# Kernel tuning notes

Measured on AMD Instinct MI355X. Metric: run time of the kernel, lower is better.

Reference implementation:

```python
import jax, jax.numpy as jnp
import numpy as np

B, L, D_IN = 8, 512, 1024
HEAD_SIZE = 64
NUM_LABELS = 16
INF = 1e12


def _rotary_sin_cos(seq_len, dim):
    # HF RoFormerSinusoidalPositionalEmbedding: inv_freq = 10000^(-2i/dim)
    pos = np.arange(seq_len, dtype=np.float64)[:, None]
    inv_freq = 1.0 / np.power(10000.0, 2.0 * np.arange(dim // 2) / dim)
    ang = pos * inv_freq  # [L, dim//2]
    # interleave: [s0, s0, s1, s1, ...] (matches stack([sin,sin],-1).reshape)
    sin = jnp.asarray(np.repeat(np.sin(ang), 2, axis=-1), dtype=jnp.float32)
    cos = jnp.asarray(np.repeat(np.cos(ang), 2, axis=-1), dtype=jnp.float32)
    return sin[None], cos[None]  # [1, L, dim]


def _rotate_half(x):
    # [-x1, x0, -x3, x2, ...]
    return jnp.stack([-x[..., 1::2], x[..., ::2]], axis=-1).reshape(x.shape)


def setup_inputs() -> dict:
    key = jax.random.key(0)
    k1, k2, k3, k4, k5 = jax.random.split(key, 5)
    s1 = 1.0 / np.sqrt(D_IN)
    s2 = 1.0 / np.sqrt(2 * HEAD_SIZE)
    return {
        "inputs": jax.random.normal(k1, (B, L, D_IN), dtype=jnp.float32),
        "attention_mask": jnp.ones((B, L), dtype=jnp.int32),
        "W1": jax.random.uniform(k2, (D_IN, 2 * HEAD_SIZE), jnp.float32, -s1, s1),
        "b1": jax.random.uniform(k3, (2 * HEAD_SIZE,), jnp.float32, -s1, s1),
        "W2": jax.random.uniform(k4, (2 * HEAD_SIZE, 2 * NUM_LABELS), jnp.float32, -s2, s2),
        "b2": jax.random.uniform(k5, (2 * NUM_LABELS,), jnp.float32, -s2, s2),
    }


def reference(inputs, attention_mask, W1, b1, W2, b2):
    h = inputs @ W1 + b1                      # [B, L, 2*head_size]
    qw, kw = h[..., ::2], h[..., 1::2]        # [B, L, head_size]

    sin, cos = _rotary_sin_cos(h.shape[1], HEAD_SIZE)
    qw = qw * cos + _rotate_half(qw) * sin
    kw = kw * cos + _rotate_half(kw) * sin

    logits = jnp.einsum("bmd,bnd->bmn", qw, kw) / (HEAD_SIZE ** 0.5)  # [B, L, L]

    bias = (h @ W2 + b2).transpose(0, 2, 1) / 2.0        # [B, 2*heads, L]
    logits = logits[:, None] + bias[:, ::2, None, :] + bias[:, 1::2, :, None]  # [B, heads, L, L]

    am = attention_mask.astype(logits.dtype)
    attn_mask = 1.0 - am[:, None, None, :] * am[:, None, :, None]
    logits = logits - attn_mask * INF

    tril = jnp.tril(jnp.ones((h.shape[1], h.shape[1]), logits.dtype), k=-1)
    logits = logits - tril * INF
    return logits
```

## Files before the change

### kernel.cpp

```cpp
#include <hip/hip_runtime.h>
#include <math.h>

#define B_   8
#define L_   512
#define DIN  1024
#define H_   128
#define HEAD 64
#define NL   16
#define INF_ 1.0e12f

#define SIN_OFF  0
#define COS_OFF  (512*32)
#define QROT_OFF (COS_OFF + 512*32)
#define KROT_OFF (QROT_OFF + B_*L_*HEAD)
#define BQ_OFF   (KROT_OFF + B_*L_*HEAD)
#define BK_OFF   (BQ_OFF + B_*NL*L_)
#define W1T_OFF  (BK_OFF + B_*NL*L_)
#define W2T_OFF  (W1T_OFF + 65536)

typedef float          floatx4  __attribute__((ext_vector_type(4)));
typedef short          shortx8  __attribute__((ext_vector_type(8)));
typedef unsigned short ushortx8 __attribute__((ext_vector_type(8)));

__device__ __forceinline__ unsigned short f2bf(float f) {
    unsigned u = __float_as_uint(f);
    u += 0x7FFFu + ((u >> 16) & 1u);
    return (unsigned short)(u >> 16);
}

__global__ __launch_bounds__(256) void prep_kernel(const float* __restrict__ W1,
                                                   const float* __restrict__ W2,
                                                   float* __restrict__ ws) {
    __shared__ float lds[64 * 132];
    const int tid = threadIdx.x;
    const int bid = blockIdx.x;

    if (bid < 64) {
        int idx = bid * 256 + tid;
        int m = idx >> 5, i = idx & 31;
        float freq = expf(-(float)i * 0.28782313662425575f);
        float ang  = (float)m * freq;
        ws[SIN_OFF + idx] = sinf(ang);
        ws[COS_OFF + idx] = cosf(ang);
    } else if (bid < 80) {
        const int k0 = (bid - 64) * 64;
        for (int i = 0; i < 8; i++) {
            int f = tid + i * 256;
            int k = f >> 5, n4 = (f & 31) * 4;
            *(float4*)&lds[k * 132 + n4] = *(const float4*)&W1[(size_t)(k0 + k) * H_ + n4];
        }
        __syncthreads();
        unsigned short* W1T = (unsigned short*)(ws + W1T_OFF);
        const int n  = tid >> 1;
        const int kh = (tid & 1) * 32;
        for (int i = 0; i < 4; i++) {
            ushortx8 p;
            #pragma unroll
            for (int j = 0; j < 8; j++) p[j] = f2bf(lds[(kh + i * 8 + j) * 132 + n]);
            *(ushortx8*)&W1T[(size_t)n * DIN + k0 + kh + i * 8] = p;
        }
    } else {
        unsigned short* W2T = (unsigned short*)(ws + W2T_OFF);
        const int o  = tid >> 3;
        const int kc = (tid & 7) * 16;
        ushortx8 p0, p1;
        #pragma unroll
        for (int j = 0; j < 8; j++) p0[j] = f2bf(W2[(size_t)(kc + j) * 32 + o]);
        #pragma unroll
        for (int j = 0; j < 8; j++) p1[j] = f2bf(W2[(size_t)(kc + 8 + j) * 32 + o]);
        *(ushortx8*)&W2T[(size_t)o * H_ + kc]     = p0;
        *(ushortx8*)&W2T[(size_t)o * H_ + kc + 8] = p1;
    }
}

__global__ __launch_bounds__(1024, 4) void gemm1_fused_kernel(
    const float* __restrict__ X, const float* __restrict__ b1,
    const float* __restrict__ b2, float* __restrict__ ws)
{
    __shared__ float red[8][16][64];
    __shared__ float hs[16 * 132];

    const int tid  = threadIdx.x;
    const int m0   = blockIdx.x * 16;
    const int w    = tid >> 6;
    const int g    = w & 3;
    const int s    = w >> 2;
    const int lane = tid & 63;
    const int lrow = lane >> 4;
    const int lcol = lane & 15;

    const unsigned short* W1T = (const unsigned short*)(ws + W1T_OFF);

    const float* pA = X + (size_t)(m0 + lcol) * DIN + s * 256 + lrow * 8;
    const unsigned short* pB0 = W1T + (size_t)(g * 32 + lcol) * DIN + s * 256 + lrow * 8;
    const unsigned short* pB1 = pB0 + (size_t)16 * DIN;

    floatx4 acc0 = {0.f, 0.f, 0.f, 0.f};
    floatx4 acc1 = {0.f, 0.f, 0.f, 0.f};

    #pragma unroll
    for (int st = 0; st < 8; st++) {
        float4 a0 = *(const float4*)(pA + st * 32);
        float4 a1 = *(const float4*)(pA + st * 32 + 4);
        shortx8 bf0 = *(const shortx8*)(pB0 + st * 32);
        shortx8 bf1 = *(const shortx8*)(pB1 + st * 32);
        ushortx8 afu;
        afu[0] = f2bf(a0.x); afu[1] = f2bf(a0.y); afu[2] = f2bf(a0.z); afu[3] = f2bf(a0.w);
        afu[4] = f2bf(a1.x); afu[5] = f2bf(a1.y); afu[6] = f2bf(a1.z); afu[7] = f2bf(a1.w);
        shortx8 af = (shortx8)afu;
        acc0 = __builtin_amdgcn_mfma_f32_16x16x32_bf16(af, bf0, acc0, 0, 0, 0);
        acc1 = __builtin_amdgcn_mfma_f32_16x16x32_bf16(af, bf1, acc1, 0, 0, 0);
    }

    #pragma unroll
    for (int r = 0; r < 4; r++) {
        red[r][w][lane]     = acc0[r];
        red[4 + r][w][lane] = acc1[r];
    }
    __syncthreads();

    if (w < 4) {
        float b1a = b1[g * 32 + lcol];
        float b1b = b1[g * 32 + 16 + lcol];
        #pragma unroll
        for (int r = 0; r < 4; r++) {
            float v0 = red[r][g][lane]     + red[r][g + 4][lane]
                     + red[r][g + 8][lane] + red[r][g + 12][lane];
            float v1 = red[4 + r][g][lane]     + red[4 + r][g + 4][lane]
                     + red[4 + r][g + 8][lane] + red[4 + r][g + 12][lane];
            hs[(lrow * 4 + r) * 132 + g * 32 + lcol]      = v0 + b1a;
            hs[(lrow * 4 + r) * 132 + g * 32 + 16 + lcol] = v1 + b1b;
        }
    }
    __syncthreads();

    if (tid < 256) {
        int row = tid >> 4;
        int j   = tid & 15;
        int gg  = m0 + row;
        int pos = gg & (L_ - 1);
        const float* hr = &hs[row * 132];
        float h0 = hr[8 * j + 0], h1 = hr[8 * j + 1];
        float h2 = hr[8 * j + 2], h3 = hr[8 * j + 3];
        float h4 = hr[8 * j + 4], h5 = hr[8 * j + 5];
        float h6 = hr[8 * j + 6], h7 = hr[8 * j + 7];
        float s0 = ws[SIN_OFF + pos * 32 + 2 * j];
        float c0 = ws[COS_OFF + pos * 32 + 2 * j];
        float s1 = ws[SIN_OFF + pos * 32 + 2 * j + 1];
        float c1 = ws[COS_OFF + pos * 32 + 2 * j + 1];
        float4 q, k;
        q.x = h0 * c0 - h2 * s0;  q.y = h2 * c0 + h0 * s0;
        q.z = h4 * c1 - h6 * s1;  q.w = h6 * c1 + h4 * s1;
        k.x = h1 * c0 - h3 * s0;  k.y = h3 * c0 + h1 * s0;
        k.z = h5 * c1 - h7 * s1;  k.w = h7 * c1 + h5 * s1;
        *(float4*)&ws[QROT_OFF + (size_t)gg * HEAD + 4 * j] = q;
        *(float4*)&ws[KROT_OFF + (size_t)gg * HEAD + 4 * j] = k;
    }

    if (w == 0) {
        const unsigned short* W2T = (const unsigned short*)(ws + W2T_OFF);
        floatx4 bacc0 = {0.f, 0.f, 0.f, 0.f};
        floatx4 bacc1 = {0.f, 0.f, 0.f, 0.f};
        #pragma unroll
        for (int st = 0; st < 4; st++) {
            int k = st * 32 + lrow * 8;
            ushortx8 hfu;
            #pragma unroll
            for (int j = 0; j < 8; j++) hfu[j] = f2bf(hs[lcol * 132 + k + j]);
            shortx8 hf = (shortx8)hfu;
            shortx8 wf0 = *(const shortx8*)(W2T + (size_t)lcol * H_ + k);
            shortx8 wf1 = *(const shortx8*)(W2T + (size_t)(16 + lcol) * H_ + k);
            bacc0 = __builtin_amdgcn_mfma_f32_16x16x32_bf16(hf, wf0, bacc0, 0, 0, 0);
            bacc1 = __builtin_amdgcn_mfma_f32_16x16x32_bf16(hf, wf1, bacc1, 0, 0, 0);
        }
        float b2a = b2[lcol], b2b = b2[16 + lcol];
        #pragma unroll
        for (int r = 0; r < 4; r++) {
            int gg  = m0 + lrow * 4 + r;
            int bb  = gg >> 9;
            int pos = gg & (L_ - 1);
            float v0 = (bacc0[r] + b2a) * 0.5f;
            float v1 = (bacc1[r] + b2b) * 0.5f;
            int o0 = lcol, o1 = 16 + lcol;
            if (o0 & 1) ws[BQ_OFF + ((size_t)bb * NL + (o0 >> 1)) * L_ + pos] = v0;
            else        ws[BK_OFF + ((size_t)bb * NL + (o0 >> 1)) * L_ + pos] = v0;
            if (o1 & 1) ws[BQ_OFF + ((size_t)bb * NL + (o1 >> 1)) * L_ + pos] = v1;
            else        ws[BK_OFF + ((size_t)bb * NL + (o1 >> 1)) * L_ + pos] = v1;
        }
    }
}

__global__ __launch_bounds__(256) void qk_bcast_kernel(
    const int* __restrict__ am, const float* __restrict__ ws, float* __restrict__ out)
{
    __shared__ float Qs[64][68];
    __shared__ float Ks[64][68];
    __shared__ float BQs[16][64];
    __shared__ float BKs[16][64];
    __shared__ float maskM[64];
    __shared__ float maskN[64];

    const int tid = threadIdx.x;
    const int bid = blockIdx.x;
    const int bb = bid >> 6;
    const int mt = (bid >> 3) & 7;
    const int nt = bid & 7;
    const int m0 = mt * 64, n0 = nt * 64;

    {
        int r0   = tid >> 4;
        int dcol = (tid & 15) * 4;
        #pragma unroll
        for (int rr = 0; rr < 4; rr++) {
            int r = r0 + rr * 16;
            float4 q = *(const float4*)&ws[QROT_OFF + ((size_t)(bb * L_ + m0 + r)) * HEAD + dcol];
            float4 k = *(const float4*)&ws[KROT_OFF + ((size_t)(bb * L_ + n0 + r)) * HEAD + dcol];
            Qs[dcol + 0][r] = q.x; Qs[dcol + 1][r] = q.y;
            Qs[dcol + 2][r] = q.z; Qs[dcol + 3][r] = q.w;
            Ks[dcol + 0][r] = k.x; Ks[dcol + 1][r] = k.y;
            Ks[dcol + 2][r] = k.z; Ks[dcol + 3][r] = k.w;
        }
    }
    {
        int l = tid >> 4;
        int c = (tid & 15) * 4;
        *(float4*)&BQs[l][c] = *(const float4*)&ws[BQ_OFF + ((size_t)bb * NL + l) * L_ + m0 + c];
        *(float4*)&BKs[l][c] = *(const float4*)&ws[BK_OFF + ((size_t)bb * NL + l) * L_ + n0 + c];
    }
    if (tid < 64)       maskM[tid]      = (float)am[bb * L_ + m0 + tid];
    else if (tid < 128) maskN[tid - 64] = (float)am[bb * L_ + n0 + (tid - 64)];
    __syncthreads();

    const int ty = tid >> 4;
    const int tx = tid & 15;
    float acc[4][4] = {};
    #pragma unroll 8
    for (int d = 0; d < HEAD; d++) {
        float4 a  = *(const float4*)&Qs[d][ty * 4];
        float4 bv = *(const float4*)&Ks[d][tx * 4];
        acc[0][0] += a.x * bv.x; acc[0][1] += a.x * bv.y; acc[0][2] += a.x * bv.z; acc[0][3] += a.x * bv.w;
        acc[1][0] += a.y * bv.x; acc[1][1] += a.y * bv.y; acc[1][2] += a.y * bv.z; acc[1][3] += a.y * bv.w;
        acc[2][0] += a.z * bv.x; acc[2][1] += a.z * bv.y; acc[2][2] += a.z * bv.z; acc[2][3] += a.z * bv.w;
        acc[3][0] += a.w * bv.x; acc[3][1] += a.w * bv.y; acc[3][2] += a.w * bv.z; acc[3][3] += a.w * bv.w;
    }

    float4 base[4];
    #pragma unroll
    for (int r = 0; r < 4; r++) {
        int m = m0 + ty * 4 + r;
        float mm = maskM[ty * 4 + r];
        #pragma unroll
        for (int c = 0; c < 4; c++) {
            int n = n0 + tx * 4 + c;
            float v = acc[r][c] * 0.125f
                    - (1.0f - mm * maskN[tx * 4 + c]) * INF_
                    - ((n < m) ? INF_ : 0.0f);
            ((float*)&base[r])[c] = v;
        }
    }

    #pragma unroll
    for (int l = 0; l < NL; l++) {
        float4 bk4 = *(const float4*)&BKs[l][tx * 4];
        size_t outb = (((size_t)(bb * NL + l)) * L_ + m0 + ty * 4) * L_ + n0 + tx * 4;
        #pragma unroll
        for (int r = 0; r < 4; r++) {
            float bq = BQs[l][ty * 4 + r];
            float4 o;
            o.x = base[r].x + bk4.x + bq;
            o.y = base[r].y + bk4.y + bq;
            o.z = base[r].z + bk4.z + bq;
            o.w = base[r].w + bk4.w + bq;
            *(float4*)&out[outb + (size_t)r * L_] = o;
        }
    }
}

extern "C" void kernel_launch(void* const* d_in, const int* in_sizes, int n_in,
                              void* d_out, int out_size, void* d_ws, size_t ws_size,
                              hipStream_t stream) {
    const float* X  = (const float*)d_in[0];
    const int*   am = (const int*)d_in[1];
    const float* W1 = (const float*)d_in[2];
    const float* b1 = (const float*)d_in[3];
    const float* W2 = (const float*)d_in[4];
    const float* b2 = (const float*)d_in[5];
    float* out = (float*)d_out;
    float* ws  = (float*)d_ws;

    prep_kernel<<<81, 256, 0, stream>>>(W1, W2, ws);
    gemm1_fused_kernel<<<(B_ * L_) / 16, 1024, 0, stream>>>(X, b1, b2, ws);
    qk_bcast_kernel<<<B_ * (L_ / 64) * (L_ / 64), 256, 0, stream>>>(am, ws, out);
}
```

Baseline: 54.01 us.

## Stage X tile through LDS as bf16 with coalesced loads and prefetched W1

The GEMM1 kernel now loads each X row with fully coalesced float4 reads (one wave per row), converts to bf16 once, and stores it into an LDS buffer that aliases the reduction scratch. It also prefetches all W1T fragments into registers before the MFMA loop. MFMA A-operands are then read from padded LDS instead of strided global loads. This removes uncoalesced global access and keeps loads in flight, at the cost of extra barriers, more registers, and a lower occupancy hint in launch_bounds.

```diff
diff --git a/kernel.cpp b/kernel.cpp
--- a/kernel.cpp
+++ b/kernel.cpp
@@ -17,6 +17,8 @@
 #define BK_OFF   (BQ_OFF + B_*NL*L_)
 #define W1T_OFF  (BK_OFF + B_*NL*L_)
 #define W2T_OFF  (W1T_OFF + 65536)
+
+#define XSH_STRIDE 1032
 
 typedef float          floatx4  __attribute__((ext_vector_type(4)));
 typedef short          shortx8  __attribute__((ext_vector_type(8)));
@@ -73,12 +75,15 @@
     }
 }
 
-__global__ __launch_bounds__(1024, 4) void gemm1_fused_kernel(
+__global__ __launch_bounds__(1024, 2) void gemm1_fused_kernel(
     const float* __restrict__ X, const float* __restrict__ b1,
     const float* __restrict__ b2, float* __restrict__ ws)
 {
-    __shared__ float red[8][16][64];
+    __shared__ __align__(16) float shbuf[8256];
     __shared__ float hs[16 * 132];
+
+    unsigned short* Xsh = (unsigned short*)shbuf;
+    float (*red)[16][64] = (float(*)[16][64])shbuf;
 
     const int tid  = threadIdx.x;
     const int m0   = blockIdx.x * 16;
@@ -91,26 +96,44 @@
 
     const unsigned short* W1T = (const unsigned short*)(ws + W1T_OFF);
 
-    const float* pA = X + (size_t)(m0 + lcol) * DIN + s * 256 + lrow * 8;
+    const float* xrow = X + (size_t)(m0 + w) * DIN + lane * 8;
+    float4 x0 = *(const float4*)(xrow + 0);
+    float4 x1 = *(const float4*)(xrow + 4);
+    float4 x2 = *(const float4*)(xrow + 512);
+    float4 x3 = *(const float4*)(xrow + 516);
+
     const unsigned short* pB0 = W1T + (size_t)(g * 32 + lcol) * DIN + s * 256 + lrow * 8;
     const unsigned short* pB1 = pB0 + (size_t)16 * DIN;
+    shortx8 bfr[16];
+    #pragma unroll
+    for (int st = 0; st < 8; st++) {
+        bfr[2 * st]     = *(const shortx8*)(pB0 + st * 32);
+        bfr[2 * st + 1] = *(const shortx8*)(pB1 + st * 32);
+    }
+
+    {
+        ushortx8 ua, ub;
+        ua[0] = f2bf(x0.x); ua[1] = f2bf(x0.y); ua[2] = f2bf(x0.z); ua[3] = f2bf(x0.w);
+        ua[4] = f2bf(x1.x); ua[5] = f2bf(x1.y); ua[6] = f2bf(x1.z); ua[7] = f2bf(x1.w);
+        ub[0] = f2bf(x2.x); ub[1] = f2bf(x2.y); ub[2] = f2bf(x2.z); ub[3] = f2bf(x2.w);
+        ub[4] = f2bf(x3.x); ub[5] = f2bf(x3.y); ub[6] = f2bf(x3.z); ub[7] = f2bf(x3.w);
+        *(ushortx8*)&Xsh[w * XSH_STRIDE + lane * 8]       = ua;
+        *(ushortx8*)&Xsh[w * XSH_STRIDE + 512 + lane * 8] = ub;
+    }
+    __syncthreads();
+
+    const unsigned short* pA = &Xsh[lcol * XSH_STRIDE + s * 256 + lrow * 8];
 
     floatx4 acc0 = {0.f, 0.f, 0.f, 0.f};
     floatx4 acc1 = {0.f, 0.f, 0.f, 0.f};
 
     #pragma unroll
     for (int st = 0; st < 8; st++) {
-        float4 a0 = *(const float4*)(pA + st * 32);
-        float4 a1 = *(const float4*)(pA + st * 32 + 4);
-        shortx8 bf0 = *(const shortx8*)(pB0 + st * 32);
-        shortx8 bf1 = *(const shortx8*)(pB1 + st * 32);
-        ushortx8 afu;
-        afu[0] = f2bf(a0.x); afu[1] = f2bf(a0.y); afu[2] = f2bf(a0.z); afu[3] = f2bf(a0.w);
-        afu[4] = f2bf(a1.x); afu[5] = f2bf(a1.y); afu[6] = f2bf(a1.z); afu[7] = f2bf(a1.w);
-        shortx8 af = (shortx8)afu;
-        acc0 = __builtin_amdgcn_mfma_f32_16x16x32_bf16(af, bf0, acc0, 0, 0, 0);
-        acc1 = __builtin_amdgcn_mfma_f32_16x16x32_bf16(af, bf1, acc1, 0, 0, 0);
-    }
+        shortx8 af = *(const shortx8*)(pA + st * 32);
+        acc0 = __builtin_amdgcn_mfma_f32_16x16x32_bf16(af, bfr[2 * st],     acc0, 0, 0, 0);
+        acc1 = __builtin_amdgcn_mfma_f32_16x16x32_bf16(af, bfr[2 * st + 1], acc1, 0, 0, 0);
+    }
+    __syncthreads();
 
     #pragma unroll
     for (int r = 0; r < 4; r++) {
```

Result: faster. 48.48 us (-10.2%).
